# Performance work log

Measured on AMD Instinct MI355X. Metric: run time of the kernel, lower is better.

## Reference

```python
import jax, jax.numpy as jnp
import numpy as np

S_DIM, A_DIM, H_DIM = 256, 18, 256
E, NS, B = 5, 10, 4096  # ensemble, MC samples, batch


def setup_inputs() -> dict:
    key = jax.random.key(0)
    ks = iter(jax.random.split(key, 40))
    def kaiming(k, shape):
        return jax.random.normal(k, shape, jnp.float32) * np.float32(np.sqrt(2.0 / shape[-1]))
    inp = {
        "state": jax.random.normal(next(ks), (B, S_DIM), jnp.float32),
        "num_samples": NS,
    }
    dims = [(H_DIM, S_DIM), (H_DIM, H_DIM), (A_DIM, H_DIM)]
    for i, (o, ii) in enumerate(dims):
        inp[f"w_mu{i}"] = kaiming(next(ks), (E, o, ii))
        inp[f"w_rho{i}"] = jnp.full((E, o, ii), -3.0, jnp.float32)
        inp[f"b_mu{i}"] = jnp.zeros((E, o), jnp.float32)
        inp[f"b_rho{i}"] = jnp.full((E, o), -3.0, jnp.float32)
        inp[f"w_eps{i}"] = jax.random.normal(next(ks), (E, NS, o, ii), jnp.float32)
        inp[f"b_eps{i}"] = jax.random.normal(next(ks), (E, NS, o), jnp.float32)
    # uncertainty head: Linear(2A->H), ReLU, Linear(H->A), Softplus
    inp["uh_w1"] = kaiming(next(ks), (H_DIM, 2 * A_DIM))
    inp["uh_b1"] = jnp.zeros((H_DIM,), jnp.float32)
    inp["uh_w2"] = kaiming(next(ks), (A_DIM, H_DIM))
    inp["uh_b2"] = jnp.zeros((A_DIM,), jnp.float32)
    # risk head: Linear(3A->H), ReLU, Linear(H->1)
    inp["rh_w1"] = kaiming(next(ks), (H_DIM, 3 * A_DIM))
    inp["rh_b1"] = jnp.zeros((H_DIM,), jnp.float32)
    inp["rh_w2"] = kaiming(next(ks), (1, H_DIM))
    inp["rh_b2"] = jnp.zeros((1,), jnp.float32)
    return inp


def _kl(mu, sigma):
    # KL(N(mu, sigma) || N(0, 1)) summed over param dims -> per-ensemble [E]
    kl = -jnp.log(sigma) + (sigma ** 2 + mu ** 2) * 0.5 - 0.5
    return jnp.sum(kl, axis=tuple(range(1, mu.ndim)))


def _bayes(x, wmu, wrho, bmu, brho, weps, beps):
    # x: [E,S,B,in]; wmu: [E,out,in]; weps: [E,S,out,in]
    wsig = jax.nn.softplus(wrho)
    bsig = jax.nn.softplus(brho)
    w = wmu[:, None] + wsig[:, None] * weps        # [E,S,out,in]
    b = bmu[:, None] + bsig[:, None] * beps        # [E,S,out]
    y = jnp.einsum('esbi,esoi->esbo', x, w) + b[:, :, None, :]
    kl = _kl(wmu, wsig) + _kl(bmu, bsig)           # [E] (same for all MC samples)
    return y, kl


def reference(state, num_samples,
              w_mu0, w_rho0, b_mu0, b_rho0, w_eps0, b_eps0,
              w_mu1, w_rho1, b_mu1, b_rho1, w_eps1, b_eps1,
              w_mu2, w_rho2, b_mu2, b_rho2, w_eps2, b_eps2,
              uh_w1, uh_b1, uh_w2, uh_b2,
              rh_w1, rh_b1, rh_w2, rh_b2):
    e, ns = w_eps0.shape[0], w_eps0.shape[1]
    x = jnp.broadcast_to(state, (e, ns) + state.shape)          # [E,S,B,in]
    x, kl0 = _bayes(x, w_mu0, w_rho0, b_mu0, b_rho0, w_eps0, b_eps0)
    x = jax.nn.relu(x)  # dropout = identity (eval)
    x, kl1 = _bayes(x, w_mu1, w_rho1, b_mu1, b_rho1, w_eps1, b_eps1)
    x = jax.nn.relu(x)
    x, kl2 = _bayes(x, w_mu2, w_rho2, b_mu2, b_rho2, w_eps2, b_eps2)
    net_out = x.mean(axis=1)                                     # [E,B,A]
    q_mean = net_out.mean(axis=0)                                # [B,A]
    q_var = jnp.var(net_out, axis=0, ddof=1)                     # unbiased, as torch .var
    epistemic = q_var
    u_in = jnp.concatenate([q_mean, q_var], axis=-1)             # [B,2A]
    h = jax.nn.relu(u_in @ uh_w1.T + uh_b1)
    aleatoric = jax.nn.softplus(h @ uh_w2.T + uh_b2)             # [B,A]
    total_unc = epistemic + aleatoric
    r_in = jnp.concatenate([q_mean, epistemic, aleatoric], axis=-1)  # [B,3A]
    risk = jax.nn.relu(r_in @ rh_w1.T + rh_b1) @ rh_w2.T + rh_b2     # [B,1]
    s = 2.0 * jnp.sqrt(total_unc)
    lcb, ucb = q_mean - s, q_mean + s
    # total_kl = sum_e ns*kl_e ; divided by (E*num_samples) -> mean over ensemble
    kl_div = jnp.sum(kl0 + kl1 + kl2) / e
    return (q_mean, epistemic, aleatoric, total_unc, lcb, ucb, risk, kl_div)
```

## Files before the change

kernel.cpp:

```cpp
#include <hip/hip_runtime.h>
#include <hip/hip_bf16.h>


typedef __bf16 bf16x8 __attribute__((ext_vector_type(8)));
typedef float f32x4 __attribute__((ext_vector_type(4)));
typedef float f32x16 __attribute__((ext_vector_type(16)));
typedef unsigned short u16x4 __attribute__((ext_vector_type(4)));
typedef unsigned short u16x8 __attribute__((ext_vector_type(8)));

__device__ __forceinline__ unsigned short f2bf(float f) {
  unsigned int u = __builtin_bit_cast(unsigned int, f);
  u += 0x7fffu + ((u >> 16) & 1u);
  return (unsigned short)(u >> 16);
}

__device__ __forceinline__ float softplus_f(float x) {
  return (x > 20.f) ? x : __logf(1.f + __expf(x));
}

__device__ __forceinline__ float klterm(float m, float sg) {
  return -__logf(sg) + (sg * sg + m * m) * 0.5f - 0.5f;
}

__device__ __forceinline__ f32x16 mfma32(bf16x8 a, bf16x8 b, f32x16 c) {
  return __builtin_amdgcn_mfma_f32_32x32x16_bf16(a, b, c, 0, 0, 0);
}


__device__ __forceinline__ void scvt_body(int gid, const float* __restrict__ s,
                                          unsigned short* __restrict__ d) {
  const f32x4* p = (const f32x4*)(s + (size_t)gid * 8);
  f32x4 x0 = p[0], x1 = p[1];
  u16x8 v = {f2bf(x0.x), f2bf(x0.y), f2bf(x0.z), f2bf(x0.w),
             f2bf(x1.x), f2bf(x1.y), f2bf(x1.z), f2bf(x1.w)};
  *(u16x8*)(d + (size_t)gid * 8) = v;
}

template <int O, int OPAD>
__device__ __forceinline__ float wgen_body(int gid, const float* __restrict__ wmu,
                                           const float* __restrict__ wrho,
                                           const float* __restrict__ weps,
                                           char* __restrict__ wf) {
  int es = gid / (OPAD * 32);
  int rem = gid - es * (OPAD * 32);
  int o = rem >> 5;
  int i8 = (rem & 31) * 8;
  int e = es / 10, s = es - e * 10;
  float v[8];
  float kl = 0.f;
  if (O == OPAD || o < O) {
    const float* mu = wmu + ((size_t)(e * O + o)) * 256 + i8;
    const float* rho = wrho + ((size_t)(e * O + o)) * 256 + i8;
    const float* eps = weps + ((size_t)((e * 10 + s) * O + o)) * 256 + i8;
    float mv[8], rv[8], ev[8];
    *(f32x4*)(mv) = ((const f32x4*)mu)[0];
    *(f32x4*)(mv + 4) = ((const f32x4*)mu)[1];
    *(f32x4*)(rv) = ((const f32x4*)rho)[0];
    *(f32x4*)(rv + 4) = ((const f32x4*)rho)[1];
    *(f32x4*)(ev) = ((const f32x4*)eps)[0];
    *(f32x4*)(ev + 4) = ((const f32x4*)eps)[1];
#pragma unroll
    for (int j = 0; j < 8; ++j) {
      float m = mv[j];
      float sg = softplus_f(rv[j]);
      v[j] = m + sg * ev[j];
      if (s == 0) kl += klterm(m, sg);
    }
  } else {
#pragma unroll
    for (int j = 0; j < 8; ++j) v[j] = 0.f;
  }
  u16x8 pk = {f2bf(v[0]), f2bf(v[1]), f2bf(v[2]), f2bf(v[3]),
              f2bf(v[4]), f2bf(v[5]), f2bf(v[6]), f2bf(v[7])};
  int osub = o >> 5, om = o & 31, kt2 = i8 >> 4, hi = (i8 >> 3) & 1;
  int lane = om + 32 * hi;
  *(u16x8*)(wf + (size_t)(((es * (OPAD / 32) + osub) * 16 + kt2) * 64 + lane) * 16) = pk;
  return kl;
}

__global__ __launch_bounds__(256) void prep_kernel(
    const float* __restrict__ state, unsigned short* __restrict__ stateb,
    const float* __restrict__ wmu0, const float* __restrict__ wrho0,
    const float* __restrict__ weps0, char* __restrict__ W0f,
    const float* __restrict__ wmu1, const float* __restrict__ wrho1,
    const float* __restrict__ weps1, char* __restrict__ W1f,
    const float* __restrict__ wmu2, const float* __restrict__ wrho2,
    const float* __restrict__ weps2, char* __restrict__ W2f,
    const float* __restrict__ bmu0, const float* __restrict__ brho0,
    const float* __restrict__ beps0, const float* __restrict__ bmu1,
    const float* __restrict__ brho1, const float* __restrict__ beps1,
    const float* __restrict__ bmu2, const float* __restrict__ brho2,
    const float* __restrict__ beps2, float* __restrict__ bias0,
    float* __restrict__ bias1, float* __restrict__ bias2,
    float* __restrict__ partials) {
  int bid = blockIdx.x, t = threadIdx.x;
  float kl = 0.f;
  if (bid < 512) {
    scvt_body(bid * 256 + t, state, stateb);
  } else if (bid < 2112) {
    kl = wgen_body<256, 256>((bid - 512) * 256 + t, wmu0, wrho0, weps0, W0f);
  } else if (bid < 3712) {
    kl = wgen_body<256, 256>((bid - 2112) * 256 + t, wmu1, wrho1, weps1, W1f);
  } else if (bid < 3912) {
    kl = wgen_body<18, 32>((bid - 3712) * 256 + t, wmu2, wrho2, weps2, W2f);
  } else {
    int gid = (bid - 3912) * 256 + t;
    if (gid < 12800) {
      int es = gid >> 8, o = gid & 255, e = es / 10, s = es - e * 10;
      float m = bmu0[e * 256 + o];
      float sg = softplus_f(brho0[e * 256 + o]);
      bias0[gid] = m + sg * beps0[(e * 10 + s) * 256 + o];
      if (s == 0) kl = klterm(m, sg);
    } else if (gid < 25600) {
      int id = gid - 12800;
      int es = id >> 8, o = id & 255, e = es / 10, s = es - e * 10;
      float m = bmu1[e * 256 + o];
      float sg = softplus_f(brho1[e * 256 + o]);
      bias1[id] = m + sg * beps1[(e * 10 + s) * 256 + o];
      if (s == 0) kl = klterm(m, sg);
    } else if (gid < 27200) {
      int id = gid - 25600;
      int es = id >> 5, o = id & 31, e = es / 10, s = es - e * 10;
      if (o < 18) {
        float m = bmu2[e * 18 + o];
        float sg = softplus_f(brho2[e * 18 + o]);
        bias2[id] = m + sg * beps2[(e * 10 + s) * 18 + o];
        if (s == 0) kl = klterm(m, sg);
      } else {
        bias2[id] = 0.f;
      }
    }
  }
#pragma unroll
  for (int m = 32; m >= 1; m >>= 1) kl += __shfl_xor(kl, m);
  __shared__ float wsum[4];
  if ((t & 63) == 0) wsum[t >> 6] = kl;
  __syncthreads();
  if (t == 0) partials[bid] = wsum[0] + wsum[1] + wsum[2] + wsum[3];
}

__device__ __forceinline__ void mlp_layer32(const char* __restrict__ wA,
                                            const float* __restrict__ bias_es,
                                            int og, char* __restrict__ buf,
                                            int lane) {
  const char* a0p = wA + (size_t)(2 * og) * 16384;
  const char* a1p = a0p + 16384;
  const char* b0p = buf;
  const char* b1p = buf + 16384;
  int lo = lane * 16;
  f32x16 acc00, acc01, acc10, acc11;
#pragma unroll
  for (int c = 0; c < 16; ++c) {
    acc00[c] = 0.f; acc01[c] = 0.f; acc10[c] = 0.f; acc11[c] = 0.f;
  }

  bf16x8 a0c = *(const bf16x8*)(a0p + lo);
  bf16x8 a1c = *(const bf16x8*)(a1p + lo);
  bf16x8 b0c = *(const bf16x8*)(b0p + lo);
  bf16x8 b1c = *(const bf16x8*)(b1p + lo);
#pragma unroll
  for (int kp = 0; kp < 8; ++kp) {
    bf16x8 a0n = *(const bf16x8*)(a0p + (2 * kp + 1) * 1024 + lo);
    bf16x8 a1n = *(const bf16x8*)(a1p + (2 * kp + 1) * 1024 + lo);
    bf16x8 b0n = *(const bf16x8*)(b0p + (2 * kp + 1) * 1024 + lo);
    bf16x8 b1n = *(const bf16x8*)(b1p + (2 * kp + 1) * 1024 + lo);
    __builtin_amdgcn_s_setprio(1);
    acc00 = mfma32(a0c, b0c, acc00);
    acc01 = mfma32(a0c, b1c, acc01);
    acc10 = mfma32(a1c, b0c, acc10);
    acc11 = mfma32(a1c, b1c, acc11);
    __builtin_amdgcn_s_setprio(0);
    if (kp < 7) {
      a0c = *(const bf16x8*)(a0p + (2 * kp + 2) * 1024 + lo);
      a1c = *(const bf16x8*)(a1p + (2 * kp + 2) * 1024 + lo);
      b0c = *(const bf16x8*)(b0p + (2 * kp + 2) * 1024 + lo);
      b1c = *(const bf16x8*)(b1p + (2 * kp + 2) * 1024 + lo);
    }
    __builtin_amdgcn_s_setprio(1);
    acc00 = mfma32(a0n, b0n, acc00);
    acc01 = mfma32(a0n, b1n, acc01);
    acc10 = mfma32(a1n, b0n, acc10);
    acc11 = mfma32(a1n, b1n, acc11);
    __builtin_amdgcn_s_setprio(0);
  }
  __syncthreads();

  int hi = lane >> 5, bcol = lane & 31;
  auto epi = [&](const f32x16& A, int i, int j) {
    int obt = og * 64 + i * 32;
    char* fb = buf + (size_t)(j * 16) * 1024;
#pragma unroll
    for (int q = 0; q < 4; ++q) {
      int o0 = obt + 8 * q + 4 * hi;
      f32x4 bv = *(const f32x4*)(bias_es + o0);
      float v0 = fmaxf(A[4 * q + 0] + bv.x, 0.f);
      float v1 = fmaxf(A[4 * q + 1] + bv.y, 0.f);
      float v2 = fmaxf(A[4 * q + 2] + bv.z, 0.f);
      float v3 = fmaxf(A[4 * q + 3] + bv.w, 0.f);
      u16x4 pk = {f2bf(v0), f2bf(v1), f2bf(v2), f2bf(v3)};
      int kt2t = o0 >> 4;
      *(u16x4*)(fb + kt2t * 1024 + (bcol + 32 * (q & 1)) * 16 + 8 * hi) = pk;
    }
  };
  epi(acc00, 0, 0);
  epi(acc01, 0, 1);
  epi(acc10, 1, 0);
  epi(acc11, 1, 1);
  __syncthreads();
}

__global__ __launch_bounds__(256, 4) void mlp_fused(
    const unsigned short* __restrict__ stateb, const char* __restrict__ W0f,
    const char* __restrict__ W1f, const char* __restrict__ W2f,
    const float* __restrict__ bias0, const float* __restrict__ bias1,
    const float* __restrict__ bias2, float* __restrict__ y2) {
  __shared__ char lds[40960];
  char* buf = lds;
  float* scratch = (float*)(lds + 32768);
  int tid = threadIdx.x, w = tid >> 6, lane = tid & 63;
  int lo = lane * 16;

  int bid = blockIdx.x;
  int lin = (bid & 7) * 400 + (bid >> 3);
  int es = lin >> 6, b0 = (lin & 63) * 64;
  int og = w;

#pragma unroll
  for (int it = 0; it < 8; ++it) {
    int F = it * 4 + w, bt = F >> 4, kt2 = F & 15;
    const unsigned short* src =
        stateb + (size_t)(b0 + bt * 32 + (lane & 31)) * 256 + kt2 * 16 + (lane >> 5) * 8;
    *(u16x8*)(buf + F * 1024 + lo) = *(const u16x8*)src;
  }
  __syncthreads();

  mlp_layer32(W0f + (size_t)es * 131072, bias0 + es * 256, og, buf, lane);
  mlp_layer32(W1f + (size_t)es * 131072, bias1 + es * 256, og, buf, lane);

  int bt2 = w & 1, kh = w >> 1;
  f32x16 acc2;
#pragma unroll
  for (int c = 0; c < 16; ++c) acc2[c] = 0.f;
  const char* b2k = buf + (size_t)bt2 * 16384 + kh * 8192;
  const char* w2p = W2f + (size_t)es * 16384 + kh * 8192;
#pragma unroll
  for (int k = 0; k < 8; ++k) {
    bf16x8 a = *(const bf16x8*)(w2p + k * 1024 + lo);
    bf16x8 bb = *(const bf16x8*)(b2k + k * 1024 + lo);
    acc2 = mfma32(a, bb, acc2);
  }
  if (kh == 1) {
#pragma unroll
    for (int q = 0; q < 4; ++q) {
      f32x4 v = {acc2[4 * q], acc2[4 * q + 1], acc2[4 * q + 2], acc2[4 * q + 3]};
      *(f32x4*)(scratch + (size_t)((bt2 * 4 + q) * 64 + lane) * 4) = v;
    }
  }
  __syncthreads();
  if (kh == 0) {
    int hi = lane >> 5, bcol = lane & 31;
    int b_idx = b0 + bt2 * 32 + bcol;
    float* yp = y2 + ((size_t)es * 4096 + b_idx) * 20;
    float s[16];
#pragma unroll
    for (int q = 0; q < 4; ++q) {
      f32x4 p = *(const f32x4*)(scratch + (size_t)((bt2 * 4 + q) * 64 + lane) * 4);
      f32x4 bv = *(const f32x4*)(bias2 + es * 32 + 8 * q + 4 * hi);
      s[4 * q + 0] = acc2[4 * q + 0] + p.x + bv.x;
      s[4 * q + 1] = acc2[4 * q + 1] + p.y + bv.y;
      s[4 * q + 2] = acc2[4 * q + 2] + p.z + bv.z;
      s[4 * q + 3] = acc2[4 * q + 3] + p.w + bv.w;
    }
    if (hi == 0) {
      f32x4 v0 = {s[0], s[1], s[2], s[3]};
      f32x4 v1 = {s[4], s[5], s[6], s[7]};
      float2 v2 = {s[8], s[9]};
      *(f32x4*)(yp) = v0;
      *(f32x4*)(yp + 8) = v1;
      *(float2*)(yp + 16) = v2;
    } else {
      f32x4 v0 = {s[0], s[1], s[2], s[3]};
      f32x4 v1 = {s[4], s[5], s[6], s[7]};
      *(f32x4*)(yp + 4) = v0;
      *(f32x4*)(yp + 12) = v1;
    }
  }
}

__global__ __launch_bounds__(256) void heads_kernel(
    const float* __restrict__ y2, const float* __restrict__ partials,
    const float* __restrict__ uh_w1, const float* __restrict__ uh_b1,
    const float* __restrict__ uh_w2, const float* __restrict__ uh_b2,
    const float* __restrict__ rh_w1, const float* __restrict__ rh_b1,
    const float* __restrict__ rh_w2, const float* __restrict__ rh_b2,
    float* __restrict__ out) {
  int bid = blockIdx.x, t = threadIdx.x;
  if (bid == 512) {
    if (t < 64) {
      float acc = 0.f;
      for (int i = t; i < 4019; i += 64) acc += partials[i];
#pragma unroll
      for (int m = 32; m >= 1; m >>= 1) acc += __shfl_xor(acc, m);
      if (t == 0) out[446464] = acc * 0.2f;
    }
    return;
  }
  int b0 = bid * 8;

  __shared__ float ysh[8][1004];
  __shared__ float qsE[8][90];
  __shared__ float rin[8][56];
  __shared__ float h[8][260];

  for (int i = t; i < 2000; i += 256) {
    int r = i / 250, c = i - r * 250;
    int es_t = c / 5, part = c - es_t * 5;
    *(f32x4*)(&ysh[r][c * 4]) =
        *(const f32x4*)(y2 + ((size_t)es_t * 4096 + b0 + r) * 20 + part * 4);
  }
  __syncthreads();

  for (int i = t; i < 720; i += 256) {
    int r = i / 90, ae = i - r * 90;
    int a = ae / 5, e = ae - a * 5;
    float v = 0.f;
#pragma unroll
    for (int s = 0; s < 10; ++s) v += ysh[r][(e * 10 + s) * 20 + a];
    qsE[r][ae] = v * 0.1f;
  }
  __syncthreads();

  if (t < 144) {
    int r = t / 18, a = t - (t / 18) * 18;
    float qs = 0.f, qq = 0.f;
#pragma unroll
    for (int e = 0; e < 5; ++e) {
      float v = qsE[r][a * 5 + e];
      qs += v;
      qq += v * v;
    }
    float mean = qs * 0.2f;
    float var = fmaxf((qq - 5.f * mean * mean) * 0.25f, 0.f);
    rin[r][a] = mean;
    rin[r][18 + a] = var;
    out[(b0 + r) * 18 + a] = mean;
    out[73728 + (b0 + r) * 18 + a] = var;
  }
  __syncthreads();

  {
    f32x4 wv[9];
    const f32x4* wr = (const f32x4*)(uh_w1 + t * 36);
#pragma unroll
    for (int j = 0; j < 9; ++j) wv[j] = wr[j];
    float bb = uh_b1[t];
#pragma unroll
    for (int r = 0; r < 8; ++r) {
      float acc = bb;
#pragma unroll
      for (int j = 0; j < 9; ++j) {
        acc += wv[j].x * rin[r][j * 4] + wv[j].y * rin[r][j * 4 + 1] +
               wv[j].z * rin[r][j * 4 + 2] + wv[j].w * rin[r][j * 4 + 3];
      }
      h[r][t] = fmaxf(acc, 0.f);
    }
  }
  __syncthreads();

  if (t < 144) {
    int r = t / 18, a = t - (t / 18) * 18;
    float p = 0.f;
    const f32x4* w2r = (const f32x4*)(uh_w2 + a * 256);
#pragma unroll
    for (int j = 0; j < 64; ++j) {
      f32x4 wv = w2r[j];
      f32x4 hv = *(const f32x4*)(&h[r][j * 4]);
      p += wv.x * hv.x + wv.y * hv.y + wv.z * hv.z + wv.w * hv.w;
    }
    float alea = softplus_f(p + uh_b2[a]);
    float qm = rin[r][a], epi = rin[r][18 + a];
    float tu = epi + alea;
    float s2 = 2.f * sqrtf(tu);
    int b = b0 + r;
    out[2 * 73728 + b * 18 + a] = alea;
    out[3 * 73728 + b * 18 + a] = tu;
    out[4 * 73728 + b * 18 + a] = qm - s2;
    out[5 * 73728 + b * 18 + a] = qm + s2;
    rin[r][36 + a] = alea;
  }
  __syncthreads();

  {
    float w1v[54];
    const float2* wr2 = (const float2*)(rh_w1 + t * 54);
#pragma unroll
    for (int j = 0; j < 27; ++j) {
      float2 wv = wr2[j];
      w1v[j * 2] = wv.x;
      w1v[j * 2 + 1] = wv.y;
    }
    float bb = rh_b1[t];
#pragma unroll
    for (int r = 0; r < 8; ++r) {
      float acc = bb;
#pragma unroll
      for (int j = 0; j < 54; ++j) acc += w1v[j] * rin[r][j];
      h[r][t] = fmaxf(acc, 0.f);
    }
  }
  __syncthreads();

  if (t < 8) {
    float p = 0.f;
    const f32x4* w2r = (const f32x4*)(rh_w2);
#pragma unroll
    for (int j = 0; j < 64; ++j) {
      f32x4 wv = w2r[j];
      f32x4 hv = *(const f32x4*)(&h[t][j * 4]);
      p += wv.x * hv.x + wv.y * hv.y + wv.z * hv.z + wv.w * hv.w;
    }
    out[6 * 73728 + b0 + t] = p + rh_b2[0];
  }
}

extern "C" void kernel_launch(void* const* d_in, const int* in_sizes, int n_in,
                              void* d_out, int out_size, void* d_ws, size_t ws_size,
                              hipStream_t stream) {
  const float* state = (const float*)d_in[0];
  const float* w_mu0 = (const float*)d_in[2];
  const float* w_rho0 = (const float*)d_in[3];
  const float* b_mu0 = (const float*)d_in[4];
  const float* b_rho0 = (const float*)d_in[5];
  const float* w_eps0 = (const float*)d_in[6];
  const float* b_eps0 = (const float*)d_in[7];
  const float* w_mu1 = (const float*)d_in[8];
  const float* w_rho1 = (const float*)d_in[9];
  const float* b_mu1 = (const float*)d_in[10];
  const float* b_rho1 = (const float*)d_in[11];
  const float* w_eps1 = (const float*)d_in[12];
  const float* b_eps1 = (const float*)d_in[13];
  const float* w_mu2 = (const float*)d_in[14];
  const float* w_rho2 = (const float*)d_in[15];
  const float* b_mu2 = (const float*)d_in[16];
  const float* b_rho2 = (const float*)d_in[17];
  const float* w_eps2 = (const float*)d_in[18];
  const float* b_eps2 = (const float*)d_in[19];
  const float* uh_w1 = (const float*)d_in[20];
  const float* uh_b1 = (const float*)d_in[21];
  const float* uh_w2 = (const float*)d_in[22];
  const float* uh_b2 = (const float*)d_in[23];
  const float* rh_w1 = (const float*)d_in[24];
  const float* rh_b1 = (const float*)d_in[25];
  const float* rh_w2 = (const float*)d_in[26];
  const float* rh_b2 = (const float*)d_in[27];
  float* out = (float*)d_out;

  char* ws = (char*)d_ws;
  unsigned short* stateb = (unsigned short*)ws;
  char* W0f = ws + 2097152;
  char* W1f = W0f + 6553600;
  char* W2f = W1f + 6553600;
  float* bias0 = (float*)(W2f + 819200);
  float* bias1 = bias0 + 12800;
  float* bias2 = bias1 + 12800;
  float* y2 = bias2 + 1600;
  float* klpart = y2 + (size_t)50 * 4096 * 20;

  prep_kernel<<<4019, 256, 0, stream>>>(
      state, stateb, w_mu0, w_rho0, w_eps0, W0f, w_mu1, w_rho1, w_eps1, W1f,
      w_mu2, w_rho2, w_eps2, W2f, b_mu0, b_rho0, b_eps0, b_mu1, b_rho1, b_eps1,
      b_mu2, b_rho2, b_eps2, bias0, bias1, bias2, klpart);
  mlp_fused<<<3200, 256, 0, stream>>>(stateb, W0f, W1f, W2f, bias0, bias1,
                                      bias2, y2);
  heads_kernel<<<513, 256, 0, stream>>>(y2, klpart, uh_w1, uh_b1, uh_w2, uh_b2,
                                        rh_w1, rh_b1, rh_w2, rh_b2, out);
}
```

Before: 105.9 us.

## Stage weight panels via LDS in prep and use 8 waves per MLP block

The prep kernel now builds each 16KB bf16 weight panel per block, staging it in shared memory and writing it out contiguously with fewer, larger blocks. Previously each thread scattered its own 16-byte fragments. The fused MLP kernel moves from 4 to 8 waves per block: each wave computes one 32-row output slice with two accumulators instead of two slices with four, and uses a deeper software-prefetch ring for its operands. This raises parallelism and lowers register pressure per wave, in exchange for more LDS traffic per FLOP and extra block-wide barriers.

```diff
diff --git a/kernel.cpp b/kernel.cpp
--- a/kernel.cpp
+++ b/kernel.cpp
@@ -26,6 +26,50 @@
   return __builtin_amdgcn_mfma_f32_32x32x16_bf16(a, b, c, 0, 0, 0);
 }
 
+template <int O>
+__device__ __forceinline__ float wpanel_body(
+    int p, int t, const float* __restrict__ wmu, const float* __restrict__ wrho,
+    const float* __restrict__ weps, char* __restrict__ wf,
+    char* __restrict__ lb) {
+  int es = (O == 256) ? (p >> 3) : p;
+  int osub = (O == 256) ? (p & 7) : 0;
+  int e = es / 10, s = es - e * 10;
+  float kl = 0.f;
+  int i = (4 * t) & 255;
+  int kt2 = i >> 4, byo = (i & 7) * 2, hi32 = 32 * ((i >> 3) & 1);
+#pragma unroll
+  for (int j = 0; j < 8; ++j) {
+    int o = j * 4 + (t >> 6);
+    int og = osub * 32 + o;
+    float v[4];
+    if (O == 256 || og < O) {
+      size_t base = ((size_t)(e * O + og)) * 256 + i;
+      f32x4 m4 = *(const f32x4*)(wmu + base);
+      f32x4 r4 = *(const f32x4*)(wrho + base);
+      f32x4 e4 = *(const f32x4*)(weps + ((size_t)((e * 10 + s) * O + og)) * 256 + i);
+#pragma unroll
+      for (int c = 0; c < 4; ++c) {
+        float m = m4[c];
+        float sg = softplus_f(r4[c]);
+        v[c] = m + sg * e4[c];
+        if (s == 0) kl += klterm(m, sg);
+      }
+    } else {
+#pragma unroll
+      for (int c = 0; c < 4; ++c) v[c] = 0.f;
+    }
+    u16x4 pk = {f2bf(v[0]), f2bf(v[1]), f2bf(v[2]), f2bf(v[3])};
+    *(u16x4*)(lb + kt2 * 1024 + (o + hi32) * 16 + byo) = pk;
+  }
+  __syncthreads();
+  char* dst = wf + (size_t)p * 16384;
+#pragma unroll
+  for (int j = 0; j < 4; ++j) {
+    int idx = j * 256 + t;
+    *(u16x8*)(dst + idx * 16) = *(const u16x8*)(lb + idx * 16);
+  }
+  return kl;
+}
 
 __device__ __forceinline__ void scvt_body(int gid, const float* __restrict__ s,
                                           unsigned short* __restrict__ d) {
@@ -34,48 +78,6 @@
   u16x8 v = {f2bf(x0.x), f2bf(x0.y), f2bf(x0.z), f2bf(x0.w),
              f2bf(x1.x), f2bf(x1.y), f2bf(x1.z), f2bf(x1.w)};
   *(u16x8*)(d + (size_t)gid * 8) = v;
-}
-
-template <int O, int OPAD>
-__device__ __forceinline__ float wgen_body(int gid, const float* __restrict__ wmu,
-                                           const float* __restrict__ wrho,
-                                           const float* __restrict__ weps,
-                                           char* __restrict__ wf) {
-  int es = gid / (OPAD * 32);
-  int rem = gid - es * (OPAD * 32);
-  int o = rem >> 5;
-  int i8 = (rem & 31) * 8;
-  int e = es / 10, s = es - e * 10;
-  float v[8];
-  float kl = 0.f;
-  if (O == OPAD || o < O) {
-    const float* mu = wmu + ((size_t)(e * O + o)) * 256 + i8;
-    const float* rho = wrho + ((size_t)(e * O + o)) * 256 + i8;
-    const float* eps = weps + ((size_t)((e * 10 + s) * O + o)) * 256 + i8;
-    float mv[8], rv[8], ev[8];
-    *(f32x4*)(mv) = ((const f32x4*)mu)[0];
-    *(f32x4*)(mv + 4) = ((const f32x4*)mu)[1];
-    *(f32x4*)(rv) = ((const f32x4*)rho)[0];
-    *(f32x4*)(rv + 4) = ((const f32x4*)rho)[1];
-    *(f32x4*)(ev) = ((const f32x4*)eps)[0];
-    *(f32x4*)(ev + 4) = ((const f32x4*)eps)[1];
-#pragma unroll
-    for (int j = 0; j < 8; ++j) {
-      float m = mv[j];
-      float sg = softplus_f(rv[j]);
-      v[j] = m + sg * ev[j];
-      if (s == 0) kl += klterm(m, sg);
-    }
-  } else {
-#pragma unroll
-    for (int j = 0; j < 8; ++j) v[j] = 0.f;
-  }
-  u16x8 pk = {f2bf(v[0]), f2bf(v[1]), f2bf(v[2]), f2bf(v[3]),
-              f2bf(v[4]), f2bf(v[5]), f2bf(v[6]), f2bf(v[7])};
-  int osub = o >> 5, om = o & 31, kt2 = i8 >> 4, hi = (i8 >> 3) & 1;
-  int lane = om + 32 * hi;
-  *(u16x8*)(wf + (size_t)(((es * (OPAD / 32) + osub) * 16 + kt2) * 64 + lane) * 16) = pk;
-  return kl;
 }
 
 __global__ __launch_bounds__(256) void prep_kernel(
@@ -93,18 +95,19 @@
     const float* __restrict__ beps2, float* __restrict__ bias0,
     float* __restrict__ bias1, float* __restrict__ bias2,
     float* __restrict__ partials) {
+  __shared__ char lb[16384];
   int bid = blockIdx.x, t = threadIdx.x;
   float kl = 0.f;
   if (bid < 512) {
     scvt_body(bid * 256 + t, state, stateb);
-  } else if (bid < 2112) {
-    kl = wgen_body<256, 256>((bid - 512) * 256 + t, wmu0, wrho0, weps0, W0f);
-  } else if (bid < 3712) {
-    kl = wgen_body<256, 256>((bid - 2112) * 256 + t, wmu1, wrho1, weps1, W1f);
-  } else if (bid < 3912) {
-    kl = wgen_body<18, 32>((bid - 3712) * 256 + t, wmu2, wrho2, weps2, W2f);
+  } else if (bid < 912) {
+    kl = wpanel_body<256>(bid - 512, t, wmu0, wrho0, weps0, W0f, lb);
+  } else if (bid < 1312) {
+    kl = wpanel_body<256>(bid - 912, t, wmu1, wrho1, weps1, W1f, lb);
+  } else if (bid < 1362) {
+    kl = wpanel_body<18>(bid - 1312, t, wmu2, wrho2, weps2, W2f, lb);
   } else {
-    int gid = (bid - 3912) * 256 + t;
+    int gid = (bid - 1362) * 256 + t;
     if (gid < 12800) {
       int es = gid >> 8, o = gid & 255, e = es / 10, s = es - e * 10;
       float m = bmu0[e * 256 + o];
@@ -139,55 +142,44 @@
   if (t == 0) partials[bid] = wsum[0] + wsum[1] + wsum[2] + wsum[3];
 }
 
-__device__ __forceinline__ void mlp_layer32(const char* __restrict__ wA,
-                                            const float* __restrict__ bias_es,
-                                            int og, char* __restrict__ buf,
-                                            int lane) {
-  const char* a0p = wA + (size_t)(2 * og) * 16384;
-  const char* a1p = a0p + 16384;
+__device__ __forceinline__ void mlp_layer32o(const char* __restrict__ wA,
+                                             const float* __restrict__ bias_es,
+                                             int og, char* __restrict__ buf,
+                                             int lane) {
+  const char* ap = wA + (size_t)og * 16384;
   const char* b0p = buf;
   const char* b1p = buf + 16384;
   int lo = lane * 16;
-  f32x16 acc00, acc01, acc10, acc11;
-#pragma unroll
-  for (int c = 0; c < 16; ++c) {
-    acc00[c] = 0.f; acc01[c] = 0.f; acc10[c] = 0.f; acc11[c] = 0.f;
-  }
-
-  bf16x8 a0c = *(const bf16x8*)(a0p + lo);
-  bf16x8 a1c = *(const bf16x8*)(a1p + lo);
-  bf16x8 b0c = *(const bf16x8*)(b0p + lo);
-  bf16x8 b1c = *(const bf16x8*)(b1p + lo);
-#pragma unroll
-  for (int kp = 0; kp < 8; ++kp) {
-    bf16x8 a0n = *(const bf16x8*)(a0p + (2 * kp + 1) * 1024 + lo);
-    bf16x8 a1n = *(const bf16x8*)(a1p + (2 * kp + 1) * 1024 + lo);
-    bf16x8 b0n = *(const bf16x8*)(b0p + (2 * kp + 1) * 1024 + lo);
-    bf16x8 b1n = *(const bf16x8*)(b1p + (2 * kp + 1) * 1024 + lo);
+  f32x16 acc0, acc1;
+#pragma unroll
+  for (int c = 0; c < 16; ++c) { acc0[c] = 0.f; acc1[c] = 0.f; }
+
+  bf16x8 afr[5], bf0[3], bf1[3];
+#pragma unroll
+  for (int i = 0; i < 4; ++i) afr[i] = *(const bf16x8*)(ap + i * 1024 + lo);
+#pragma unroll
+  for (int i = 0; i < 3; ++i) {
+    bf0[i] = *(const bf16x8*)(b0p + i * 1024 + lo);
+    bf1[i] = *(const bf16x8*)(b1p + i * 1024 + lo);
+  }
+#pragma unroll
+  for (int kt = 0; kt < 16; ++kt) {
+    if (kt + 4 < 16) afr[(kt + 4) % 5] = *(const bf16x8*)(ap + (kt + 4) * 1024 + lo);
+    if (kt + 3 < 16) {
+      bf0[(kt + 3) % 3] = *(const bf16x8*)(b0p + (kt + 3) * 1024 + lo);
+      bf1[(kt + 3) % 3] = *(const bf16x8*)(b1p + (kt + 3) * 1024 + lo);
+    }
     __builtin_amdgcn_s_setprio(1);
-    acc00 = mfma32(a0c, b0c, acc00);
-    acc01 = mfma32(a0c, b1c, acc01);
-    acc10 = mfma32(a1c, b0c, acc10);
-    acc11 = mfma32(a1c, b1c, acc11);
+    acc0 = mfma32(afr[kt % 5], bf0[kt % 3], acc0);
+    acc1 = mfma32(afr[kt % 5], bf1[kt % 3], acc1);
     __builtin_amdgcn_s_setprio(0);
-    if (kp < 7) {
-      a0c = *(const bf16x8*)(a0p + (2 * kp + 2) * 1024 + lo);
-      a1c = *(const bf16x8*)(a1p + (2 * kp + 2) * 1024 + lo);
-      b0c = *(const bf16x8*)(b0p + (2 * kp + 2) * 1024 + lo);
-      b1c = *(const bf16x8*)(b1p + (2 * kp + 2) * 1024 + lo);
-    }
-    __builtin_amdgcn_s_setprio(1);
-    acc00 = mfma32(a0n, b0n, acc00);
-    acc01 = mfma32(a0n, b1n, acc01);
-    acc10 = mfma32(a1n, b0n, acc10);
-    acc11 = mfma32(a1n, b1n, acc11);
-    __builtin_amdgcn_s_setprio(0);
-  }
-  __syncthreads();
-
-  int hi = lane >> 5, bcol = lane & 31;
-  auto epi = [&](const f32x16& A, int i, int j) {
-    int obt = og * 64 + i * 32;
+  }
+  __syncthreads();
+
+  int hi = lane >> 5, bcol = lane & 15 | (lane & 31);
+  bcol = lane & 31;
+  auto epi = [&](const f32x16& A, int j) {
+    int obt = og * 32;
     char* fb = buf + (size_t)(j * 16) * 1024;
 #pragma unroll
     for (int q = 0; q < 4; ++q) {
@@ -202,14 +194,12 @@
       *(u16x4*)(fb + kt2t * 1024 + (bcol + 32 * (q & 1)) * 16 + 8 * hi) = pk;
     }
   };
-  epi(acc00, 0, 0);
-  epi(acc01, 0, 1);
-  epi(acc10, 1, 0);
-  epi(acc11, 1, 1);
-  __syncthreads();
-}
-
-__global__ __launch_bounds__(256, 4) void mlp_fused(
+  epi(acc0, 0);
+  epi(acc1, 1);
+  __syncthreads();
+}
+
+__global__ __launch_bounds__(512, 4) void mlp_fused(
     const unsigned short* __restrict__ stateb, const char* __restrict__ W0f,
     const char* __restrict__ W1f, const char* __restrict__ W2f,
     const float* __restrict__ bias0, const float* __restrict__ bias1,
@@ -223,41 +213,42 @@
   int bid = blockIdx.x;
   int lin = (bid & 7) * 400 + (bid >> 3);
   int es = lin >> 6, b0 = (lin & 63) * 64;
-  int og = w;
-
-#pragma unroll
-  for (int it = 0; it < 8; ++it) {
-    int F = it * 4 + w, bt = F >> 4, kt2 = F & 15;
+
+#pragma unroll
+  for (int it = 0; it < 4; ++it) {
+    int F = it * 8 + w, bt = F >> 4, kt2 = F & 15;
     const unsigned short* src =
         stateb + (size_t)(b0 + bt * 32 + (lane & 31)) * 256 + kt2 * 16 + (lane >> 5) * 8;
     *(u16x8*)(buf + F * 1024 + lo) = *(const u16x8*)src;
   }
   __syncthreads();
 
-  mlp_layer32(W0f + (size_t)es * 131072, bias0 + es * 256, og, buf, lane);
-  mlp_layer32(W1f + (size_t)es * 131072, bias1 + es * 256, og, buf, lane);
-
-  int bt2 = w & 1, kh = w >> 1;
+  mlp_layer32o(W0f + (size_t)es * 131072, bias0 + es * 256, w, buf, lane);
+  mlp_layer32o(W1f + (size_t)es * 131072, bias1 + es * 256, w, buf, lane);
+
+  int bt2 = w & 1, kh = (w >> 1) & 1;
   f32x16 acc2;
 #pragma unroll
   for (int c = 0; c < 16; ++c) acc2[c] = 0.f;
-  const char* b2k = buf + (size_t)bt2 * 16384 + kh * 8192;
-  const char* w2p = W2f + (size_t)es * 16384 + kh * 8192;
-#pragma unroll
-  for (int k = 0; k < 8; ++k) {
-    bf16x8 a = *(const bf16x8*)(w2p + k * 1024 + lo);
-    bf16x8 bb = *(const bf16x8*)(b2k + k * 1024 + lo);
-    acc2 = mfma32(a, bb, acc2);
-  }
-  if (kh == 1) {
-#pragma unroll
-    for (int q = 0; q < 4; ++q) {
-      f32x4 v = {acc2[4 * q], acc2[4 * q + 1], acc2[4 * q + 2], acc2[4 * q + 3]};
-      *(f32x4*)(scratch + (size_t)((bt2 * 4 + q) * 64 + lane) * 4) = v;
-    }
-  }
-  __syncthreads();
-  if (kh == 0) {
+  if (w < 4) {
+    const char* b2k = buf + (size_t)bt2 * 16384 + kh * 8192;
+    const char* w2p = W2f + (size_t)es * 16384 + kh * 8192;
+#pragma unroll
+    for (int k = 0; k < 8; ++k) {
+      bf16x8 a = *(const bf16x8*)(w2p + k * 1024 + lo);
+      bf16x8 bb = *(const bf16x8*)(b2k + k * 1024 + lo);
+      acc2 = mfma32(a, bb, acc2);
+    }
+    if (kh == 1) {
+#pragma unroll
+      for (int q = 0; q < 4; ++q) {
+        f32x4 v = {acc2[4 * q], acc2[4 * q + 1], acc2[4 * q + 2], acc2[4 * q + 3]};
+        *(f32x4*)(scratch + (size_t)((bt2 * 4 + q) * 64 + lane) * 4) = v;
+      }
+    }
+  }
+  __syncthreads();
+  if (w < 4 && kh == 0) {
     int hi = lane >> 5, bcol = lane & 31;
     int b_idx = b0 + bt2 * 32 + bcol;
     float* yp = y2 + ((size_t)es * 4096 + b_idx) * 20;
@@ -298,7 +289,7 @@
   if (bid == 512) {
     if (t < 64) {
       float acc = 0.f;
-      for (int i = t; i < 4019; i += 64) acc += partials[i];
+      for (int i = t; i < 1469; i += 64) acc += partials[i];
 #pragma unroll
       for (int m = 32; m >= 1; m >>= 1) acc += __shfl_xor(acc, m);
       if (t == 0) out[446464] = acc * 0.2f;
@@ -466,11 +457,11 @@
   float* y2 = bias2 + 1600;
   float* klpart = y2 + (size_t)50 * 4096 * 20;
 
-  prep_kernel<<<4019, 256, 0, stream>>>(
+  prep_kernel<<<1469, 256, 0, stream>>>(
       state, stateb, w_mu0, w_rho0, w_eps0, W0f, w_mu1, w_rho1, w_eps1, W1f,
       w_mu2, w_rho2, w_eps2, W2f, b_mu0, b_rho0, b_eps0, b_mu1, b_rho1, b_eps1,
       b_mu2, b_rho2, b_eps2, bias0, bias1, bias2, klpart);
-  mlp_fused<<<3200, 256, 0, stream>>>(stateb, W0f, W1f, W2f, bias0, bias1,
+  mlp_fused<<<3200, 512, 0, stream>>>(stateb, W0f, W1f, W2f, bias0, bias1,
                                       bias2, y2);
   heads_kernel<<<513, 256, 0, stream>>>(y2, klpart, uh_w1, uh_b1, uh_w2, uh_b2,
                                         rh_w1, rh_b1, rh_w2, rh_b2, out);
```

After: 113.0 us. 6.6% more time.
